# Optimization experiments

Measured on AMD Instinct MI355X. Metric: run time of the kernel, lower is better.

## Reference

```python
import jax, jax.numpy as jnp
import numpy as np

C = 64
N_H = 4
N_WIN = 16
WIN_L = 8   # compressor window length (overlapped)
WIN_S = 4   # compressor stride -> T//4 blocks


def _rms(x, eps=1e-6):
    return x * jax.lax.rsqrt(jnp.mean(x * x, axis=-1, keepdims=True) + eps)


def _rope(x, negate=False):
    # x: (..., L, D); rotate-half RoPE over positions 0..L-1
    L, D = x.shape[-2], x.shape[-1]
    half = D // 2
    inv_freq = 1.0 / (10000.0 ** (jnp.arange(half, dtype=x.dtype) / half))
    ang = jnp.arange(L, dtype=x.dtype)[:, None] * inv_freq  # (L, half)
    if negate:
        ang = -ang
    cos, sin = jnp.cos(ang), jnp.sin(ang)
    x1, x2 = x[..., :half], x[..., half:]
    return jnp.concatenate([x1 * cos - x2 * sin, x1 * sin + x2 * cos], axis=-1)


def _compress(H, W):
    # overlapped token compressor: windows of WIN_L, stride WIN_S, zero-pad tail
    B, T, d = H.shape
    Tc = T // WIN_S
    Hp = jnp.pad(H, ((0, 0), (0, WIN_L - WIN_S), (0, 0)))
    idx = WIN_S * jnp.arange(Tc)[:, None] + jnp.arange(WIN_L)[None, :]  # (Tc, WIN_L)
    win = Hp[:, idx]                       # (B, Tc, WIN_L, d)
    return win.reshape(B, Tc, WIN_L * d) @ W  # (B, Tc, out)


def setup_inputs() -> dict:
    key = jax.random.key(0)
    ks = jax.random.split(key, 11)
    B, T, d = 2, 2048, 256

    def w(k, shape, fan):
        return jax.random.normal(k, shape, jnp.float32) / np.float32(np.sqrt(fan))

    H = jax.random.normal(ks[0], (B, T, d), jnp.float32)
    return {
        'H': H,
        'Wc_comp': w(ks[1], (WIN_L * d, C), WIN_L * d),
        'Wc_idx': w(ks[2], (WIN_L * d, 32), WIN_L * d),
        'W_DQ': w(ks[3], (d, 64), d),
        'W_IUQ': w(ks[4], (64, 4 * 32), 64),
        'W_w': w(ks[5], (64, 4), 64),
        'W_Q': w(ks[6], (d, N_H * C), d),
        'W_KV': w(ks[7], (d, C), d),
        'g_q': jnp.ones((N_H, C), jnp.float32),
        'g_k': jnp.ones((C,), jnp.float32),
        'g_v': jnp.ones((C,), jnp.float32),
        'Wg0': w(ks[8], (2 * C, 64), 2 * C),
        'bg0': jnp.zeros((64,), jnp.float32),
        'Wg1': w(ks[9], (2 * C, 64), 2 * C),
        'bg1': jnp.zeros((64,), jnp.float32),
        'Wout': w(ks[10], (128, d), 128),
        'bout': jnp.zeros((d,), jnp.float32),
    }


def reference(H, Wc_comp, Wc_idx, W_DQ, W_IUQ, W_w, W_Q, W_KV,
              g_q, g_k, g_v, Wg0, bg0, Wg1, bg1, Wout, bout):
    B, T, d = H.shape
    Tc = T // 4
    k_top = min(8, Tc)

    # ---- lightning indexer ----
    H_dc = H @ W_DQ                                   # (B,T,64)
    Q_I = (H_dc @ W_IUQ).reshape(B, T, 4, 32)         # (B,T,4,32)
    W_Iw = (H_dc @ W_w)[..., None]                    # (B,T,4,1)
    K_I = _compress(H, Wc_idx)                        # (B,Tc,32)
    dot = jnp.einsum('bthc,bsc->bths', Q_I, K_I)      # (B,T,4,Tc)
    I_ts = (W_Iw * jax.nn.relu(dot)).sum(axis=2)      # (B,T,Tc)

    t = jnp.arange(T)[:, None]
    s = jnp.arange(Tc)[None, :]
    mask_I = jnp.where(4 * s <= t, 0.0, -jnp.inf)     # (T,Tc) causal over blocks
    _, topk_idx = jax.lax.top_k(I_ts + mask_I, k_top)  # (B,T,k)
    bI = jnp.arange(B)[:, None, None]
    tI = jnp.arange(T)[None, :, None]
    M_comp = jnp.full((B, T, Tc), -jnp.inf).at[bI, tI, topk_idx].set(0.0)

    # ---- compressed + sliding KV ----
    KV = jnp.concatenate([_compress(H, Wc_comp), H @ W_KV], axis=1)  # (B,Tc+T,C)

    Q = (H @ W_Q).reshape(B, T, N_H, C).transpose(0, 2, 1, 3)        # (B,nh,T,C)
    Q = _rms(Q) * g_q[None, :, None, :]
    K = _rms(KV) * g_k
    V = _rms(KV) * g_v
    Q = _rope(Q)
    K = _rope(K)
    V = _rope(V)

    S = jnp.einsum('bhtc,bsc->bhts', Q, K) / np.float32(np.sqrt(C))  # (B,nh,T,Tc+T)

    S_comp = S[..., :Tc] + M_comp[:, None]
    rel = t - jnp.arange(T)[None, :]
    mask_slide = jnp.where((rel >= 0) & (rel < N_WIN), 0.0, -jnp.inf)  # (T,T)
    S_slide = S[..., Tc:] + mask_slide

    P = jax.nn.softmax(jnp.concatenate([S_comp, S_slide], axis=-1), axis=-1)
    O = jnp.einsum('bhts,bsc->bhtc', P, V)            # (B,nh,T,C)
    O = _rope(O, negate=True)

    O0 = O[:, :2].transpose(0, 2, 1, 3).reshape(B, T, 2 * C)
    O1 = O[:, 2:].transpose(0, 2, 1, 3).reshape(B, T, 2 * C)
    p_all = jnp.concatenate([O0 @ Wg0 + bg0, O1 @ Wg1 + bg1], axis=-1)
    return p_all @ Wout + bout
```

## Files before the change

kernel.cpp:

```cpp
#include <hip/hip_runtime.h>
#include <math.h>

#define T_DIM 2048
#define B_DIM 2
#define D_DIM 256
#define TC 512
#define KV_LEN 2560

__device__ __forceinline__ float wave_sum64(float v) {
#pragma unroll
    for (int off = 32; off > 0; off >>= 1) v += __shfl_xor(v, off, 64);
    return v;
}

__device__ __forceinline__ float rope_angle(int pos, int j) {
    float inv = powf(10000.0f, -(float)j * (1.0f / 32.0f));
    return (float)pos * inv;
}

__global__ __launch_bounds__(256) void k_phase1(
    const float* __restrict__ H, const float* __restrict__ W_Q,
    const float* __restrict__ W_KV, const float* __restrict__ W_DQ,
    const float* __restrict__ W_IUQ, const float* __restrict__ W_w,
    const float* __restrict__ Wc_comp, const float* __restrict__ Wc_idx,
    const float* __restrict__ g_q, const float* __restrict__ g_k,
    const float* __restrict__ g_v,
    float* __restrict__ QI, float* __restrict__ Wiw, float* __restrict__ Qr,
    float* __restrict__ KIbuf, float* __restrict__ Kbuf, float* __restrict__ Vbuf)
{
    __shared__ float smem[8960];
    int tid = threadIdx.x;
    int lane = tid & 63;

    if (blockIdx.x < 512) {
        int bt0 = blockIdx.x * 8;
        float* sH = smem;
        float* sW = smem + 2048;
        float* sHdc = smem + 8192;
        float* sWw = smem + 8704;

        for (int i = tid; i < 512; i += 256) {
            int tok = i >> 6;
            int c4 = (i & 63) << 2;
            *(float4*)&sH[tok * 256 + c4] =
                *(const float4*)(H + ((size_t)(bt0 + tok) << 8) + c4);
        }

        int cg = lane;
        int tg = tid >> 6;
        float acc[2][6];
#pragma unroll
        for (int a = 0; a < 2; ++a)
#pragma unroll
            for (int m = 0; m < 6; ++m) acc[a][m] = 0.f;

        for (int kc = 0; kc < 16; ++kc) {
            __syncthreads();
            for (int i = tid; i < 1536; i += 256) {
                int r = i / 96;
                int cc = (i % 96) * 4;
                int gr = kc * 16 + r;
                float4 v;
                if (cc < 256)      v = *(const float4*)(W_Q + (size_t)gr * 256 + cc);
                else if (cc < 320) v = *(const float4*)(W_KV + (size_t)gr * 64 + (cc - 256));
                else               v = *(const float4*)(W_DQ + (size_t)gr * 64 + (cc - 320));
                *(float4*)&sW[r * 384 + cc] = v;
            }
            __syncthreads();
#pragma unroll
            for (int k = 0; k < 16; ++k) {
                float h0 = sH[(2 * tg) * 256 + kc * 16 + k];
                float h1 = sH[(2 * tg + 1) * 256 + kc * 16 + k];
#pragma unroll
                for (int m = 0; m < 6; ++m) {
                    float w = sW[k * 384 + cg + 64 * m];
                    acc[0][m] = fmaf(h0, w, acc[0][m]);
                    acc[1][m] = fmaf(h1, w, acc[1][m]);
                }
            }
        }

#pragma unroll
        for (int tt = 0; tt < 2; ++tt)
            sHdc[(2 * tg + tt) * 64 + lane] = acc[tt][5];
        __syncthreads();
        for (int i = tid * 4; i < 8192; i += 1024)
            *(float4*)&smem[i] = *(const float4*)(W_IUQ + i);
        if (tid < 64) ((float4*)sWw)[tid] = ((const float4*)W_w)[tid];
        __syncthreads();
        float* sWI = smem;

        int j = lane & 31;
#pragma unroll
        for (int tt = 0; tt < 2; ++tt) {
            int tok = 2 * tg + tt;
            int bt = bt0 + tok;
            int b = bt >> 11;
            int t = bt & 2047;

            float s_t, c_t;
            sincosf(rope_angle(t, j), &s_t, &c_t);

#pragma unroll
            for (int r = 0; r < 4; ++r) {
                float qv = acc[tt][r];
                float ss = wave_sum64(qv * qv);
                float sc = rsqrtf(ss * (1.0f / 64.0f) + 1e-6f);
                float q = qv * sc * g_q[r * 64 + lane];
                float prt = __shfl_xor(q, 32, 64);
                float o = (lane < 32) ? fmaf(q, c_t, -prt * s_t)
                                      : fmaf(prt, s_t, q * c_t);
                Qr[(size_t)bt * 256 + r * 64 + lane] = o;
            }
            {
                float kvv = acc[tt][4];
                float ss = wave_sum64(kvv * kvv);
                float sc = rsqrtf(ss * (1.0f / 64.0f) + 1e-6f);
                float kk = kvv * sc * g_k[lane];
                float vv = kvv * sc * g_v[lane];
                int pos = TC + t;
                float s_p, c_p;
                sincosf(rope_angle(pos, j), &s_p, &c_p);
                float pk = __shfl_xor(kk, 32, 64);
                float pv = __shfl_xor(vv, 32, 64);
                float ko = (lane < 32) ? fmaf(kk, c_p, -pk * s_p) : fmaf(pk, s_p, kk * c_p);
                float vo = (lane < 32) ? fmaf(vv, c_p, -pv * s_p) : fmaf(pv, s_p, vv * c_p);
                size_t off = ((size_t)b * KV_LEN + pos) * 64 + lane;
                Kbuf[off] = ko;
                Vbuf[off] = vo;
            }
            {
                float a0 = 0.f, a1 = 0.f;
#pragma unroll 8
                for (int jj = 0; jj < 64; ++jj) {
                    float hv = sHdc[tok * 64 + jj];
                    a0 = fmaf(hv, sWI[jj * 128 + lane], a0);
                    a1 = fmaf(hv, sWI[jj * 128 + 64 + lane], a1);
                }
                QI[(size_t)bt * 128 + lane] = a0;
                QI[(size_t)bt * 128 + 64 + lane] = a1;
                if (lane < 4) {
                    float aw = 0.f;
                    for (int jj = 0; jj < 64; ++jj)
                        aw = fmaf(sHdc[tok * 64 + jj], sWw[jj * 4 + lane], aw);
                    Wiw[(size_t)bt * 4 + lane] = aw;
                }
            }
        }
    } else {
        int cid = blockIdx.x - 512;
        int wv = tid >> 6;
        int b = cid >> 8;
        int s0 = (cid & 255) * 2;

        float* sA = smem;
        float* sRed = smem + 4096;
        float* sRedI = smem + 4608;

#pragma unroll
        for (int tt = 0; tt < 2; ++tt) {
#pragma unroll
            for (int rl = 0; rl < 2; ++rl) {
                int row = 4 * (s0 + tt) + 2 * wv + rl;
                float4 v = make_float4(0.f, 0.f, 0.f, 0.f);
                if (row < T_DIM)
                    v = *(const float4*)(H + ((size_t)b * T_DIM + row) * 256 + lane * 4);
                *(float4*)&sA[(tt * 4 + wv) * 512 + rl * 256 + lane * 4] = v;
            }
        }

        int k0 = wv * 512;
        float ac0 = 0.f, ac1 = 0.f;
        const float* Wc = Wc_comp + (size_t)k0 * 64 + lane;
        for (int k = 0; k < 512; k += 4) {
            float4 a0 = *(float4*)&sA[(0 * 4 + wv) * 512 + k];
            float4 a1 = *(float4*)&sA[(1 * 4 + wv) * 512 + k];
#pragma unroll
            for (int kk = 0; kk < 4; ++kk) {
                float w = Wc[(size_t)(k + kk) * 64];
                ac0 = fmaf(((const float*)&a0)[kk], w, ac0);
                ac1 = fmaf(((const float*)&a1)[kk], w, ac1);
            }
        }
        sRed[(wv * 2 + 0) * 64 + lane] = ac0;
        sRed[(wv * 2 + 1) * 64 + lane] = ac1;

        {
            int col = lane & 31;
            int half = lane >> 5;
            float ai0 = 0.f, ai1 = 0.f;
            const float* Wi = Wc_idx + (size_t)k0 * 32 + col;
            int kb = half * 256;
            for (int k = kb; k < kb + 256; k += 4) {
                float4 a0 = *(float4*)&sA[(0 * 4 + wv) * 512 + k];
                float4 a1 = *(float4*)&sA[(1 * 4 + wv) * 512 + k];
#pragma unroll
                for (int kk = 0; kk < 4; ++kk) {
                    float w = Wi[(size_t)(k + kk) * 32];
                    ai0 = fmaf(((const float*)&a0)[kk], w, ai0);
                    ai1 = fmaf(((const float*)&a1)[kk], w, ai1);
                }
            }
            ai0 += __shfl_xor(ai0, 32, 64);
            ai1 += __shfl_xor(ai1, 32, 64);
            if (lane < 32) {
                sRedI[(wv * 2 + 0) * 32 + lane] = ai0;
                sRedI[(wv * 2 + 1) * 32 + lane] = ai1;
            }
        }
        __syncthreads();

        if (wv < 2) {
            int tt = wv;
            int s = s0 + tt;
            float kvv = sRed[(0 * 2 + tt) * 64 + lane] + sRed[(1 * 2 + tt) * 64 + lane] +
                        sRed[(2 * 2 + tt) * 64 + lane] + sRed[(3 * 2 + tt) * 64 + lane];
            float ss = wave_sum64(kvv * kvv);
            float sc = rsqrtf(ss * (1.0f / 64.0f) + 1e-6f);
            float kk = kvv * sc * g_k[lane];
            float vv = kvv * sc * g_v[lane];
            int j = lane & 31;
            float sa, ca;
            sincosf(rope_angle(s, j), &sa, &ca);
            float pk = __shfl_xor(kk, 32, 64);
            float pv = __shfl_xor(vv, 32, 64);
            float ko = (lane < 32) ? fmaf(kk, ca, -pk * sa) : fmaf(pk, sa, kk * ca);
            float vo = (lane < 32) ? fmaf(vv, ca, -pv * sa) : fmaf(pv, sa, vv * ca);
            size_t off = ((size_t)b * KV_LEN + s) * 64 + lane;
            Kbuf[off] = ko;
            Vbuf[off] = vo;
        } else {
            int tt = wv - 2;
            int s = s0 + tt;
            if (lane < 32) {
                float a = sRedI[(0 * 2 + tt) * 32 + lane] + sRedI[(1 * 2 + tt) * 32 + lane] +
                          sRedI[(2 * 2 + tt) * 32 + lane] + sRedI[(3 * 2 + tt) * 32 + lane];
                KIbuf[((size_t)b * TC + s) * 32 + lane] = a;
            }
        }
    }
}

__global__ __launch_bounds__(256) void k_score_topk(
    const float* __restrict__ QI, const float* __restrict__ Wiw,
    const float* __restrict__ KIbuf, int* __restrict__ topk)
{
    int tid = threadIdx.x;
    int wv = tid >> 6;
    int lane = tid & 63;
    int bt0 = blockIdx.x * 4;
    int bt = bt0 + wv;
    int b = bt >> 11;
    int t = bt & 2047;

    __shared__ float sQ[4][128];
    __shared__ float sw[4][4];
    __shared__ float sKI[64 * 33];

    sQ[wv][lane] = QI[(size_t)bt * 128 + lane];
    sQ[wv][64 + lane] = QI[(size_t)bt * 128 + 64 + lane];
    if (lane < 4) sw[wv][lane] = Wiw[(size_t)bt * 4 + lane];

    const float* KIb = KIbuf + (size_t)b * TC * 32;
    int smax = t >> 2;
    int smax_blk = ((bt0 + 3) & 2047) >> 2;

    float vals[8];
#pragma unroll
    for (int r = 0; r < 8; ++r) vals[r] = -INFINITY;

    for (int r = 0; r < 8; ++r) {
        if (r * 64 > smax_blk) break;
        __syncthreads();
        for (int i = tid; i < 512; i += 256) {
            int row = i >> 3;
            int cseg = (i & 7) * 4;
            float4 v = *(const float4*)(KIb + (size_t)(r * 64 + row) * 32 + cseg);
            float* dst = &sKI[row * 33 + cseg];
            dst[0] = v.x; dst[1] = v.y; dst[2] = v.z; dst[3] = v.w;
        }
        __syncthreads();

        int s = r * 64 + lane;
        if (s <= smax) {
            float dd0 = 0.f, dd1 = 0.f, dd2 = 0.f, dd3 = 0.f;
#pragma unroll
            for (int c = 0; c < 32; ++c) {
                float kv = sKI[lane * 33 + c];
                dd0 = fmaf(sQ[wv][c], kv, dd0);
                dd1 = fmaf(sQ[wv][32 + c], kv, dd1);
                dd2 = fmaf(sQ[wv][64 + c], kv, dd2);
                dd3 = fmaf(sQ[wv][96 + c], kv, dd3);
            }
            vals[r] = sw[wv][0] * fmaxf(dd0, 0.f) + sw[wv][1] * fmaxf(dd1, 0.f) +
                      sw[wv][2] * fmaxf(dd2, 0.f) + sw[wv][3] * fmaxf(dd3, 0.f);
        }
    }

    unsigned consumed = 0u;
    for (int k2 = 0; k2 < 8; ++k2) {
        float bv = -INFINITY;
        int bi = 0x7fffffff;
#pragma unroll
        for (int r = 0; r < 8; ++r) {
            if (!(consumed & (1u << r))) {
                int s = lane + 64 * r;
                float v = vals[r];
                if (v > bv || (v == bv && s < bi)) { bv = v; bi = s; }
            }
        }
#pragma unroll
        for (int off = 1; off < 64; off <<= 1) {
            float ov = __shfl_xor(bv, off, 64);
            int oi = __shfl_xor(bi, off, 64);
            if (ov > bv || (ov == bv && oi < bi)) { bv = ov; bi = oi; }
        }
        if ((bi & 63) == lane) consumed |= 1u << (bi >> 6);
        if (lane == 0) topk[(size_t)bt * 8 + k2] = bi;
    }
}

__global__ __launch_bounds__(1024) void k_attn_out(
    const float* __restrict__ Qr, const float* __restrict__ Kbuf,
    const float* __restrict__ Vbuf, const int* __restrict__ topk,
    const float* __restrict__ Wg0, const float* __restrict__ bg0,
    const float* __restrict__ Wg1, const float* __restrict__ bg1,
    const float* __restrict__ Wout, const float* __restrict__ bout,
    float* __restrict__ out)
{
    int tid = threadIdx.x;
    int lt = tid >> 8;
    int t256 = tid & 255;
    int h = t256 >> 6;
    int lane = tid & 63;
    int bt = blockIdx.x * 4 + lt;
    int b = bt >> 11;
    int t = bt & 2047;

    __shared__ float sKV[4][48 * 65];
    __shared__ float sQ[4][256];
    __shared__ int sPos[4][24];
    __shared__ float sP[4][4][24];
    __shared__ float sO[4][256];
    __shared__ float sPall[4][128];

    sQ[lt][t256] = Qr[(size_t)bt * 256 + t256];
    if (t256 < 8) {
        sPos[lt][t256] = topk[(size_t)bt * 8 + t256];
    } else if (t256 < 24) {
        int rel = t256 - 8;
        int sp = t - rel;
        sPos[lt][t256] = (sp >= 0) ? (TC + sp) : -1;
    }
    __syncthreads();

    for (int i = t256; i < 768; i += 256) {
        int row = i >> 4;
        int seg = (i & 15) << 2;
        int key = (row < 24) ? row : row - 24;
        int pos = sPos[lt][key];
        if (pos >= 0) {
            const float* src = ((row < 24) ? Kbuf : Vbuf) +
                               ((size_t)b * KV_LEN + pos) * 64 + seg;
            float4 v = *(const float4*)src;
            float* dst = &sKV[lt][row * 65 + seg];
            dst[0] = v.x; dst[1] = v.y; dst[2] = v.z; dst[3] = v.w;
        }
    }
    __syncthreads();

    float scv = -INFINITY;
    if (lane < 24) {
        int pos = sPos[lt][lane];
        if (pos >= 0) {
            float dd = 0.f;
#pragma unroll
            for (int c = 0; c < 64; ++c)
                dd = fmaf(sQ[lt][h * 64 + c], sKV[lt][lane * 65 + c], dd);
            scv = dd * 0.125f;
        }
    }
    float m = scv;
#pragma unroll
    for (int off = 1; off < 64; off <<= 1) m = fmaxf(m, __shfl_xor(m, off, 64));
    float p = expf(scv - m);
    if (scv == -INFINITY) p = 0.f;
    float l = p;
#pragma unroll
    for (int off = 1; off < 64; off <<= 1) l += __shfl_xor(l, off, 64);
    p /= l;
    if (lane < 24) sP[lt][h][lane] = p;

    float o = 0.f;
#pragma unroll
    for (int j2 = 0; j2 < 24; ++j2) {
        int pos = sPos[lt][j2];
        if (pos >= 0)
            o = fmaf(sP[lt][h][j2], sKV[lt][(24 + j2) * 65 + lane], o);
    }

    int j = lane & 31;
    float sa, ca;
    sincosf(rope_angle(t, j), &sa, &ca);
    float prt = __shfl_xor(o, 32, 64);
    float oo = (lane < 32) ? fmaf(o, ca, prt * sa) : fmaf(-prt, sa, o * ca);
    sO[lt][h * 64 + lane] = oo;
    __syncthreads();

    if (t256 < 128) {
        float a;
        if (t256 < 64) {
            a = bg0[t256];
            for (int c = 0; c < 128; ++c) a = fmaf(sO[lt][c], Wg0[c * 64 + t256], a);
        } else {
            int i = t256 - 64;
            a = bg1[i];
            for (int c = 0; c < 128; ++c) a = fmaf(sO[lt][128 + c], Wg1[c * 64 + i], a);
        }
        sPall[lt][t256] = a;
    }
    __syncthreads();

    float a = bout[t256];
    for (int i = 0; i < 128; ++i) a = fmaf(sPall[lt][i], Wout[i * 256 + t256], a);
    out[(size_t)bt * 256 + t256] = a;
}

extern "C" void kernel_launch(void* const* d_in, const int* in_sizes, int n_in,
                              void* d_out, int out_size, void* d_ws, size_t ws_size,
                              hipStream_t stream) {
    const float* H       = (const float*)d_in[0];
    const float* Wc_comp = (const float*)d_in[1];
    const float* Wc_idx  = (const float*)d_in[2];
    const float* W_DQ    = (const float*)d_in[3];
    const float* W_IUQ   = (const float*)d_in[4];
    const float* W_w     = (const float*)d_in[5];
    const float* W_Q     = (const float*)d_in[6];
    const float* W_KV    = (const float*)d_in[7];
    const float* g_q     = (const float*)d_in[8];
    const float* g_k     = (const float*)d_in[9];
    const float* g_v     = (const float*)d_in[10];
    const float* Wg0     = (const float*)d_in[11];
    const float* bg0     = (const float*)d_in[12];
    const float* Wg1     = (const float*)d_in[13];
    const float* bg1     = (const float*)d_in[14];
    const float* Wout    = (const float*)d_in[15];
    const float* bout    = (const float*)d_in[16];

    float* ws  = (float*)d_ws;
    float* QI  = ws;
    float* Qr  = QI + 524288;
    float* Wiw = Qr + 1048576;
    float* KI  = Wiw + 16384;
    float* Kb  = KI + 32768;
    float* Vb  = Kb + 327680;
    int* topkb = (int*)(Vb + 327680);

    float* outp = (float*)d_out;

    hipLaunchKernelGGL(k_phase1, dim3(1024), dim3(256), 0, stream,
                       H, W_Q, W_KV, W_DQ, W_IUQ, W_w, Wc_comp, Wc_idx,
                       g_q, g_k, g_v, QI, Wiw, Qr, KI, Kb, Vb);
    hipLaunchKernelGGL(k_score_topk, dim3((B_DIM * T_DIM) / 4), dim3(256), 0, stream,
                       QI, Wiw, KI, topkb);
    hipLaunchKernelGGL(k_attn_out, dim3((B_DIM * T_DIM) / 4), dim3(1024), 0, stream,
                       Qr, Kb, Vb, topkb, Wg0, bg0, Wg1, bg1, Wout, bout, outp);
}
```

Before: 213.1 us.

## Process 16 tokens per phase-1 block and 4 compressed rows per compressor block

```diff
diff --git a/kernel.cpp b/kernel.cpp
--- a/kernel.cpp
+++ b/kernel.cpp
@@ -28,29 +28,28 @@
     float* __restrict__ QI, float* __restrict__ Wiw, float* __restrict__ Qr,
     float* __restrict__ KIbuf, float* __restrict__ Kbuf, float* __restrict__ Vbuf)
 {
-    __shared__ float smem[8960];
+    __shared__ float smem[12544];
     int tid = threadIdx.x;
     int lane = tid & 63;
-
-    if (blockIdx.x < 512) {
-        int bt0 = blockIdx.x * 8;
-        float* sH = smem;
-        float* sW = smem + 2048;
-        float* sHdc = smem + 8192;
-        float* sWw = smem + 8704;
-
-        for (int i = tid; i < 512; i += 256) {
-            int tok = i >> 6;
-            int c4 = (i & 63) << 2;
-            *(float4*)&sH[tok * 256 + c4] =
-                *(const float4*)(H + ((size_t)(bt0 + tok) << 8) + c4);
-        }
-
-        int cg = lane;
-        int tg = tid >> 6;
-        float acc[2][6];
-#pragma unroll
-        for (int a = 0; a < 2; ++a)
+    int wv = tid >> 6;
+
+    if (blockIdx.x < 256) {
+        int bt0 = blockIdx.x * 16;
+        float* sHT = smem;
+        float* sW  = smem + 5120;
+        float* sHdc = smem + 11264;
+        float* sWw = smem + 12288;
+
+#pragma unroll 4
+        for (int it = 0; it < 16; ++it) {
+            float v = H[((size_t)(bt0 + it)) * 256 + tid];
+            sHT[tid * 20 + it] = v;
+        }
+
+        int l = lane, tg = wv;
+        float acc[4][6];
+#pragma unroll
+        for (int a = 0; a < 4; ++a)
 #pragma unroll
             for (int m = 0; m < 6; ++m) acc[a][m] = 0.f;
 
@@ -69,20 +68,86 @@
             __syncthreads();
 #pragma unroll
             for (int k = 0; k < 16; ++k) {
-                float h0 = sH[(2 * tg) * 256 + kc * 16 + k];
-                float h1 = sH[(2 * tg + 1) * 256 + kc * 16 + k];
-#pragma unroll
-                for (int m = 0; m < 6; ++m) {
-                    float w = sW[k * 384 + cg + 64 * m];
-                    acc[0][m] = fmaf(h0, w, acc[0][m]);
-                    acc[1][m] = fmaf(h1, w, acc[1][m]);
+                float4 h4 = *(float4*)&sHT[(kc * 16 + k) * 20 + 4 * tg];
+                float2 w0 = *(float2*)&sW[k * 384 + 2 * l];
+                float2 w1 = *(float2*)&sW[k * 384 + 128 + 2 * l];
+                float2 w2 = *(float2*)&sW[k * 384 + 256 + 2 * l];
+                const float* hp = (const float*)&h4;
+#pragma unroll
+                for (int tt = 0; tt < 4; ++tt) {
+                    float h = hp[tt];
+                    acc[tt][0] = fmaf(h, w0.x, acc[tt][0]);
+                    acc[tt][1] = fmaf(h, w0.y, acc[tt][1]);
+                    acc[tt][2] = fmaf(h, w1.x, acc[tt][2]);
+                    acc[tt][3] = fmaf(h, w1.y, acc[tt][3]);
+                    acc[tt][4] = fmaf(h, w2.x, acc[tt][4]);
+                    acc[tt][5] = fmaf(h, w2.y, acc[tt][5]);
                 }
             }
         }
 
-#pragma unroll
-        for (int tt = 0; tt < 2; ++tt)
-            sHdc[(2 * tg + tt) * 64 + lane] = acc[tt][5];
+        int il = l & 31;
+        int half_hi = l >> 5;
+#pragma unroll
+        for (int tt = 0; tt < 4; ++tt) {
+            int tok = 4 * tg + tt;
+            int bt = bt0 + tok;
+            int b = bt >> 11;
+            int t = bt & 2047;
+            int j0 = 2 * (il & 15), j1 = j0 + 1;
+            float s0, c0, s1, c1;
+            sincosf(rope_angle(t, j0), &s0, &c0);
+            sincosf(rope_angle(t, j1), &s1, &c1);
+
+#pragma unroll
+            for (int mg = 0; mg < 2; ++mg) {
+                int h = mg * 2 + half_hi;
+                float a = acc[tt][2 * mg], bb = acc[tt][2 * mg + 1];
+                float ss = a * a + bb * bb;
+#pragma unroll
+                for (int off = 1; off <= 16; off <<= 1) ss += __shfl_xor(ss, off, 64);
+                float sc = rsqrtf(ss * (1.0f / 64.0f) + 1e-6f);
+                float qa = a * sc * g_q[h * 64 + 2 * il];
+                float qb = bb * sc * g_q[h * 64 + 2 * il + 1];
+                float pa = __shfl_xor(qa, 16, 64);
+                float pb = __shfl_xor(qb, 16, 64);
+                float oa, ob;
+                if (il < 16) { oa = fmaf(qa, c0, -pa * s0); ob = fmaf(qb, c1, -pb * s1); }
+                else         { oa = fmaf(pa, s0, qa * c0);  ob = fmaf(pb, s1, qb * c1); }
+                *(float2*)&Qr[(size_t)bt * 256 + h * 64 + 2 * il] = make_float2(oa, ob);
+            }
+
+            if (l < 32) {
+                float a = acc[tt][4], bb = acc[tt][5];
+                float ss = a * a + bb * bb;
+#pragma unroll
+                for (int off = 1; off <= 16; off <<= 1) ss += __shfl_xor(ss, off, 64);
+                float sc = rsqrtf(ss * (1.0f / 64.0f) + 1e-6f);
+                float ka = a * sc * g_k[2 * il], kb = bb * sc * g_k[2 * il + 1];
+                float va = a * sc * g_v[2 * il], vb = bb * sc * g_v[2 * il + 1];
+                int pos = TC + t;
+                float s0p, c0p, s1p, c1p;
+                sincosf(rope_angle(pos, j0), &s0p, &c0p);
+                sincosf(rope_angle(pos, j1), &s1p, &c1p);
+                float pka = __shfl_xor(ka, 16, 64), pkb = __shfl_xor(kb, 16, 64);
+                float pva = __shfl_xor(va, 16, 64), pvb = __shfl_xor(vb, 16, 64);
+                float koa, kob, voa, vob;
+                if (il < 16) {
+                    koa = fmaf(ka, c0p, -pka * s0p); kob = fmaf(kb, c1p, -pkb * s1p);
+                    voa = fmaf(va, c0p, -pva * s0p); vob = fmaf(vb, c1p, -pvb * s1p);
+                } else {
+                    koa = fmaf(pka, s0p, ka * c0p);  kob = fmaf(pkb, s1p, kb * c1p);
+                    voa = fmaf(pva, s0p, va * c0p);  vob = fmaf(pvb, s1p, vb * c1p);
+                }
+                size_t off2 = ((size_t)b * KV_LEN + pos) * 64 + 2 * il;
+                *(float2*)&Kbuf[off2] = make_float2(koa, kob);
+                *(float2*)&Vbuf[off2] = make_float2(voa, vob);
+            } else {
+                sHdc[tok * 64 + 2 * (l - 32)] = acc[tt][4];
+                sHdc[tok * 64 + 2 * (l - 32) + 1] = acc[tt][5];
+            }
+        }
+
         __syncthreads();
         for (int i = tid * 4; i < 8192; i += 1024)
             *(float4*)&smem[i] = *(const float4*)(W_IUQ + i);
@@ -90,75 +155,37 @@
         __syncthreads();
         float* sWI = smem;
 
-        int j = lane & 31;
-#pragma unroll
-        for (int tt = 0; tt < 2; ++tt) {
-            int tok = 2 * tg + tt;
+#pragma unroll
+        for (int tt = 0; tt < 4; ++tt) {
+            int tok = 4 * tg + tt;
             int bt = bt0 + tok;
-            int b = bt >> 11;
-            int t = bt & 2047;
-
-            float s_t, c_t;
-            sincosf(rope_angle(t, j), &s_t, &c_t);
-
-#pragma unroll
-            for (int r = 0; r < 4; ++r) {
-                float qv = acc[tt][r];
-                float ss = wave_sum64(qv * qv);
-                float sc = rsqrtf(ss * (1.0f / 64.0f) + 1e-6f);
-                float q = qv * sc * g_q[r * 64 + lane];
-                float prt = __shfl_xor(q, 32, 64);
-                float o = (lane < 32) ? fmaf(q, c_t, -prt * s_t)
-                                      : fmaf(prt, s_t, q * c_t);
-                Qr[(size_t)bt * 256 + r * 64 + lane] = o;
-            }
-            {
-                float kvv = acc[tt][4];
-                float ss = wave_sum64(kvv * kvv);
-                float sc = rsqrtf(ss * (1.0f / 64.0f) + 1e-6f);
-                float kk = kvv * sc * g_k[lane];
-                float vv = kvv * sc * g_v[lane];
-                int pos = TC + t;
-                float s_p, c_p;
-                sincosf(rope_angle(pos, j), &s_p, &c_p);
-                float pk = __shfl_xor(kk, 32, 64);
-                float pv = __shfl_xor(vv, 32, 64);
-                float ko = (lane < 32) ? fmaf(kk, c_p, -pk * s_p) : fmaf(pk, s_p, kk * c_p);
-                float vo = (lane < 32) ? fmaf(vv, c_p, -pv * s_p) : fmaf(pv, s_p, vv * c_p);
-                size_t off = ((size_t)b * KV_LEN + pos) * 64 + lane;
-                Kbuf[off] = ko;
-                Vbuf[off] = vo;
-            }
-            {
-                float a0 = 0.f, a1 = 0.f;
+            float a0 = 0.f, a1 = 0.f;
 #pragma unroll 8
-                for (int jj = 0; jj < 64; ++jj) {
-                    float hv = sHdc[tok * 64 + jj];
-                    a0 = fmaf(hv, sWI[jj * 128 + lane], a0);
-                    a1 = fmaf(hv, sWI[jj * 128 + 64 + lane], a1);
-                }
-                QI[(size_t)bt * 128 + lane] = a0;
-                QI[(size_t)bt * 128 + 64 + lane] = a1;
-                if (lane < 4) {
-                    float aw = 0.f;
-                    for (int jj = 0; jj < 64; ++jj)
-                        aw = fmaf(sHdc[tok * 64 + jj], sWw[jj * 4 + lane], aw);
-                    Wiw[(size_t)bt * 4 + lane] = aw;
-                }
+            for (int jj = 0; jj < 64; ++jj) {
+                float hv = sHdc[tok * 64 + jj];
+                a0 = fmaf(hv, sWI[jj * 128 + l], a0);
+                a1 = fmaf(hv, sWI[jj * 128 + 64 + l], a1);
+            }
+            QI[(size_t)bt * 128 + l] = a0;
+            QI[(size_t)bt * 128 + 64 + l] = a1;
+            if (l < 4) {
+                float aw = 0.f;
+                for (int jj = 0; jj < 64; ++jj)
+                    aw = fmaf(sHdc[tok * 64 + jj], sWw[jj * 4 + l], aw);
+                Wiw[(size_t)bt * 4 + l] = aw;
             }
         }
     } else {
-        int cid = blockIdx.x - 512;
-        int wv = tid >> 6;
-        int b = cid >> 8;
-        int s0 = (cid & 255) * 2;
+        int cid = blockIdx.x - 256;
+        int b = cid >> 7;
+        int s0 = (cid & 127) * 4;
 
         float* sA = smem;
-        float* sRed = smem + 4096;
-        float* sRedI = smem + 4608;
-
-#pragma unroll
-        for (int tt = 0; tt < 2; ++tt) {
+        float* sRed = smem + 8192;
+        float* sRedI = smem + 9216;
+
+#pragma unroll
+        for (int tt = 0; tt < 4; ++tt) {
 #pragma unroll
             for (int rl = 0; rl < 2; ++rl) {
                 int row = 4 * (s0 + tt) + 2 * wv + rl;
@@ -170,51 +197,58 @@
         }
 
         int k0 = wv * 512;
-        float ac0 = 0.f, ac1 = 0.f;
+        float ac[4] = {0.f, 0.f, 0.f, 0.f};
         const float* Wc = Wc_comp + (size_t)k0 * 64 + lane;
         for (int k = 0; k < 512; k += 4) {
             float4 a0 = *(float4*)&sA[(0 * 4 + wv) * 512 + k];
             float4 a1 = *(float4*)&sA[(1 * 4 + wv) * 512 + k];
+            float4 a2 = *(float4*)&sA[(2 * 4 + wv) * 512 + k];
+            float4 a3 = *(float4*)&sA[(3 * 4 + wv) * 512 + k];
 #pragma unroll
             for (int kk = 0; kk < 4; ++kk) {
                 float w = Wc[(size_t)(k + kk) * 64];
-                ac0 = fmaf(((const float*)&a0)[kk], w, ac0);
-                ac1 = fmaf(((const float*)&a1)[kk], w, ac1);
-            }
-        }
-        sRed[(wv * 2 + 0) * 64 + lane] = ac0;
-        sRed[(wv * 2 + 1) * 64 + lane] = ac1;
+                ac[0] = fmaf(((const float*)&a0)[kk], w, ac[0]);
+                ac[1] = fmaf(((const float*)&a1)[kk], w, ac[1]);
+                ac[2] = fmaf(((const float*)&a2)[kk], w, ac[2]);
+                ac[3] = fmaf(((const float*)&a3)[kk], w, ac[3]);
+            }
+        }
+#pragma unroll
+        for (int tt = 0; tt < 4; ++tt) sRed[(wv * 4 + tt) * 64 + lane] = ac[tt];
 
         {
             int col = lane & 31;
             int half = lane >> 5;
-            float ai0 = 0.f, ai1 = 0.f;
+            float ai[4] = {0.f, 0.f, 0.f, 0.f};
             const float* Wi = Wc_idx + (size_t)k0 * 32 + col;
             int kb = half * 256;
             for (int k = kb; k < kb + 256; k += 4) {
                 float4 a0 = *(float4*)&sA[(0 * 4 + wv) * 512 + k];
                 float4 a1 = *(float4*)&sA[(1 * 4 + wv) * 512 + k];
+                float4 a2 = *(float4*)&sA[(2 * 4 + wv) * 512 + k];
+                float4 a3 = *(float4*)&sA[(3 * 4 + wv) * 512 + k];
 #pragma unroll
                 for (int kk = 0; kk < 4; ++kk) {
                     float w = Wi[(size_t)(k + kk) * 32];
-                    ai0 = fmaf(((const float*)&a0)[kk], w, ai0);
-                    ai1 = fmaf(((const float*)&a1)[kk], w, ai1);
+                    ai[0] = fmaf(((const float*)&a0)[kk], w, ai[0]);
+                    ai[1] = fmaf(((const float*)&a1)[kk], w, ai[1]);
+                    ai[2] = fmaf(((const float*)&a2)[kk], w, ai[2]);
+                    ai[3] = fmaf(((const float*)&a3)[kk], w, ai[3]);
                 }
             }
-            ai0 += __shfl_xor(ai0, 32, 64);
-            ai1 += __shfl_xor(ai1, 32, 64);
-            if (lane < 32) {
-                sRedI[(wv * 2 + 0) * 32 + lane] = ai0;
-                sRedI[(wv * 2 + 1) * 32 + lane] = ai1;
+#pragma unroll
+            for (int tt = 0; tt < 4; ++tt) {
+                ai[tt] += __shfl_xor(ai[tt], 32, 64);
+                if (lane < 32) sRedI[(wv * 4 + tt) * 32 + lane] = ai[tt];
             }
         }
         __syncthreads();
 
-        if (wv < 2) {
+        {
             int tt = wv;
             int s = s0 + tt;
-            float kvv = sRed[(0 * 2 + tt) * 64 + lane] + sRed[(1 * 2 + tt) * 64 + lane] +
-                        sRed[(2 * 2 + tt) * 64 + lane] + sRed[(3 * 2 + tt) * 64 + lane];
+            float kvv = sRed[(0 * 4 + tt) * 64 + lane] + sRed[(1 * 4 + tt) * 64 + lane] +
+                        sRed[(2 * 4 + tt) * 64 + lane] + sRed[(3 * 4 + tt) * 64 + lane];
             float ss = wave_sum64(kvv * kvv);
             float sc = rsqrtf(ss * (1.0f / 64.0f) + 1e-6f);
             float kk = kvv * sc * g_k[lane];
@@ -229,12 +263,9 @@
             size_t off = ((size_t)b * KV_LEN + s) * 64 + lane;
             Kbuf[off] = ko;
             Vbuf[off] = vo;
-        } else {
-            int tt = wv - 2;
-            int s = s0 + tt;
             if (lane < 32) {
-                float a = sRedI[(0 * 2 + tt) * 32 + lane] + sRedI[(1 * 2 + tt) * 32 + lane] +
-                          sRedI[(2 * 2 + tt) * 32 + lane] + sRedI[(3 * 2 + tt) * 32 + lane];
+                float a = sRedI[(0 * 4 + tt) * 32 + lane] + sRedI[(1 * 4 + tt) * 32 + lane] +
+                          sRedI[(2 * 4 + tt) * 32 + lane] + sRedI[(3 * 4 + tt) * 32 + lane];
                 KIbuf[((size_t)b * TC + s) * 32 + lane] = a;
             }
         }
@@ -458,7 +489,7 @@
 
     float* outp = (float*)d_out;
 
-    hipLaunchKernelGGL(k_phase1, dim3(1024), dim3(256), 0, stream,
+    hipLaunchKernelGGL(k_phase1, dim3(512), dim3(256), 0, stream,
                        H, W_Q, W_KV, W_DQ, W_IUQ, W_w, Wc_comp, Wc_idx,
                        g_q, g_k, g_v, QI, Wiw, Qr, KI, Kb, Vb);
     hipLaunchKernelGGL(k_score_topk, dim3((B_DIM * T_DIM) / 4), dim3(256), 0, stream,
```

Measured after the change: 215.6 us. About the same (+1.1%).

## Run projection and compressor GEMMs on bf16 MFMA with split-precision operands

Applied to the files above, without the earlier changes.

```diff
diff --git a/kernel.cpp b/kernel.cpp
--- a/kernel.cpp
+++ b/kernel.cpp
@@ -1,4 +1,5 @@
 #include <hip/hip_runtime.h>
+#include <hip/hip_bf16.h>
 #include <math.h>
 
 #define T_DIM 2048
@@ -6,6 +7,10 @@
 #define D_DIM 256
 #define TC 512
 #define KV_LEN 2560
+#define HPAD 2056
+
+typedef __attribute__((ext_vector_type(8))) short bf16x8;
+typedef __attribute__((ext_vector_type(4))) float f32x4;
 
 __device__ __forceinline__ float wave_sum64(float v) {
 #pragma unroll
@@ -18,226 +23,279 @@
     return (float)pos * inv;
 }
 
-__global__ __launch_bounds__(256) void k_phase1(
+__device__ __forceinline__ unsigned short f2bf_hi(float x) {
+    __hip_bfloat16 h = __float2bfloat16(x);
+    return *(unsigned short*)&h;
+}
+
+__global__ __launch_bounds__(256) void k_prep(
     const float* __restrict__ H, const float* __restrict__ W_Q,
     const float* __restrict__ W_KV, const float* __restrict__ W_DQ,
-    const float* __restrict__ W_IUQ, const float* __restrict__ W_w,
     const float* __restrict__ Wc_comp, const float* __restrict__ Wc_idx,
-    const float* __restrict__ g_q, const float* __restrict__ g_k,
+    unsigned short* __restrict__ Hp_hi, unsigned short* __restrict__ Hp_lo,
+    unsigned short* __restrict__ Bpt, unsigned short* __restrict__ Bct)
+{
+    int gtid = blockIdx.x * 256 + threadIdx.x;
+    int gstride = gridDim.x * 256;
+
+    for (int i = gtid; i < B_DIM * HPAD * 256; i += gstride) {
+        int b = i / (HPAD * 256);
+        int rem = i - b * (HPAD * 256);
+        int row = rem >> 8;
+        int col = rem & 255;
+        float x = (row < T_DIM) ? H[((size_t)b * T_DIM + row) * 256 + col] : 0.f;
+        unsigned short hi = f2bf_hi(x);
+        __hip_bfloat16 hb = *(__hip_bfloat16*)&hi;
+        float hif = __bfloat162float(hb);
+        unsigned short lo = f2bf_hi(x - hif);
+        Hp_hi[i] = hi;
+        Hp_lo[i] = lo;
+    }
+
+    for (int i = gtid; i < 384 * 768; i += gstride) {
+        int n = i / 768;
+        int kp = i - n * 768;
+        int k = kp & 255;
+        float w;
+        if (n < 256)      w = W_Q[(size_t)k * 256 + n];
+        else if (n < 320) w = W_KV[(size_t)k * 64 + (n - 256)];
+        else              w = W_DQ[(size_t)k * 64 + (n - 320)];
+        unsigned short hi = f2bf_hi(w);
+        __hip_bfloat16 hb = *(__hip_bfloat16*)&hi;
+        unsigned short lo = f2bf_hi(w - __bfloat162float(hb));
+        Bpt[i] = (kp >= 256 && kp < 512) ? lo : hi;
+    }
+
+    for (int i = gtid; i < 96 * 6144; i += gstride) {
+        int n = i / 6144;
+        int kp = i - n * 6144;
+        int k = kp & 2047;
+        float w = (n < 64) ? Wc_comp[(size_t)k * 64 + n]
+                           : Wc_idx[(size_t)k * 32 + (n - 64)];
+        unsigned short hi = f2bf_hi(w);
+        __hip_bfloat16 hb = *(__hip_bfloat16*)&hi;
+        unsigned short lo = f2bf_hi(w - __bfloat162float(hb));
+        Bct[i] = (kp >= 2048 && kp < 4096) ? lo : hi;
+    }
+}
+
+__global__ __launch_bounds__(256) void k_mfma(
+    const unsigned short* __restrict__ Hp_hi, const unsigned short* __restrict__ Hp_lo,
+    const unsigned short* __restrict__ Bpt, const unsigned short* __restrict__ Bct,
+    float* __restrict__ Pre, float* __restrict__ Prec_part)
+{
+    int tid = threadIdx.x;
+    int w = tid >> 6;
+    int lane = tid & 63;
+    int mrow = lane & 15;
+    int q = lane >> 4;
+
+    if (blockIdx.x < 64) {
+        int bt0 = blockIdx.x * 64;
+        int b = bt0 >> 11;
+        int t0 = bt0 & 2047;
+        int n0 = w * 96;
+
+        f32x4 acc[4][6];
+#pragma unroll
+        for (int mt = 0; mt < 4; ++mt)
+#pragma unroll
+            for (int nt = 0; nt < 6; ++nt) acc[mt][nt] = (f32x4){0.f, 0.f, 0.f, 0.f};
+
+        const size_t abase = (size_t)(b * HPAD + t0 + mrow) * 256;
+
+        for (int ks = 0; ks < 24; ++ks) {
+            int seg = ks >> 3;
+            int kk = 32 * (ks & 7) + 8 * q;
+            const unsigned short* Asrc = (seg < 2 ? Hp_hi : Hp_lo);
+            int kp = 32 * ks + 8 * q;
+
+            bf16x8 af[4];
+#pragma unroll
+            for (int mt = 0; mt < 4; ++mt)
+                af[mt] = *(const bf16x8*)(Asrc + abase + (size_t)(16 * mt) * 256 + kk);
+            bf16x8 bfb[6];
+#pragma unroll
+            for (int nt = 0; nt < 6; ++nt)
+                bfb[nt] = *(const bf16x8*)(Bpt + (size_t)(n0 + 16 * nt + mrow) * 768 + kp);
+#pragma unroll
+            for (int mt = 0; mt < 4; ++mt)
+#pragma unroll
+                for (int nt = 0; nt < 6; ++nt)
+                    acc[mt][nt] = __builtin_amdgcn_mfma_f32_16x16x32_bf16(
+                        af[mt], bfb[nt], acc[mt][nt], 0, 0, 0);
+        }
+
+#pragma unroll
+        for (int mt = 0; mt < 4; ++mt)
+#pragma unroll
+            for (int nt = 0; nt < 6; ++nt)
+#pragma unroll
+                for (int reg = 0; reg < 4; ++reg)
+                    Pre[(size_t)(bt0 + 16 * mt + 4 * q + reg) * 384 + n0 + 16 * nt + mrow] =
+                        acc[mt][nt][reg];
+    } else {
+        int cid = blockIdx.x - 64;
+        int m0 = cid * 64;
+        int b = m0 >> 9;
+        int s0 = m0 & 511;
+        int kw = w * 1536;
+
+        f32x4 acc[4][6];
+#pragma unroll
+        for (int mt = 0; mt < 4; ++mt)
+#pragma unroll
+            for (int nt = 0; nt < 6; ++nt) acc[mt][nt] = (f32x4){0.f, 0.f, 0.f, 0.f};
+
+        for (int ks = 0; ks < 48; ++ks) {
+            int kp = kw + 32 * ks + 8 * q;
+            int seg = kp >> 11;
+            int kk = kp & 2047;
+            int row_off = kk >> 8;
+            int kcol = kk & 255;
+            const unsigned short* Asrc = (seg < 2 ? Hp_hi : Hp_lo);
+
+            bf16x8 af[4];
+#pragma unroll
+            for (int mt = 0; mt < 4; ++mt) {
+                int m = s0 + 16 * mt + mrow;
+                af[mt] = *(const bf16x8*)(Asrc + (size_t)(b * HPAD + 4 * m + row_off) * 256 + kcol);
+            }
+            bf16x8 bfb[6];
+#pragma unroll
+            for (int nt = 0; nt < 6; ++nt)
+                bfb[nt] = *(const bf16x8*)(Bct + (size_t)(16 * nt + mrow) * 6144 + kp);
+#pragma unroll
+            for (int mt = 0; mt < 4; ++mt)
+#pragma unroll
+                for (int nt = 0; nt < 6; ++nt)
+                    acc[mt][nt] = __builtin_amdgcn_mfma_f32_16x16x32_bf16(
+                        af[mt], bfb[nt], acc[mt][nt], 0, 0, 0);
+        }
+
+        float* dst = Prec_part + (size_t)w * (1024 * 96);
+#pragma unroll
+        for (int mt = 0; mt < 4; ++mt)
+#pragma unroll
+            for (int nt = 0; nt < 6; ++nt)
+#pragma unroll
+                for (int reg = 0; reg < 4; ++reg)
+                    dst[(size_t)(m0 + 16 * mt + 4 * q + reg) * 96 + 16 * nt + mrow] =
+                        acc[mt][nt][reg];
+    }
+}
+
+__global__ __launch_bounds__(256) void k_epi_proj(
+    const float* __restrict__ Pre, const float* __restrict__ W_IUQ,
+    const float* __restrict__ W_w, const float* __restrict__ g_q,
+    const float* __restrict__ g_k, const float* __restrict__ g_v,
+    float* __restrict__ QI, float* __restrict__ Wiw, float* __restrict__ Qr,
+    float* __restrict__ Kbuf, float* __restrict__ Vbuf)
+{
+    int tid = threadIdx.x;
+    int wv = tid >> 6;
+    int lane = tid & 63;
+    int bt = blockIdx.x * 4 + wv;
+    int b = bt >> 11;
+    int t = bt & 2047;
+
+    __shared__ float sWI[8192];
+    __shared__ float sWw[256];
+    __shared__ float sHdc[4][64];
+
+    for (int i = tid * 4; i < 8192; i += 1024)
+        *(float4*)&sWI[i] = *(const float4*)(W_IUQ + i);
+    if (tid < 64) ((float4*)sWw)[tid] = ((const float4*)W_w)[tid];
+
+    const float* pr = Pre + (size_t)bt * 384;
+    sHdc[wv][lane] = pr[320 + lane];
+    __syncthreads();
+
+    int j = lane & 31;
+    float s_t, c_t;
+    sincosf(rope_angle(t, j), &s_t, &c_t);
+
+#pragma unroll
+    for (int r = 0; r < 4; ++r) {
+        float qv = pr[r * 64 + lane];
+        float ss = wave_sum64(qv * qv);
+        float sc = rsqrtf(ss * (1.0f / 64.0f) + 1e-6f);
+        float qq = qv * sc * g_q[r * 64 + lane];
+        float prt = __shfl_xor(qq, 32, 64);
+        float o = (lane < 32) ? fmaf(qq, c_t, -prt * s_t)
+                              : fmaf(prt, s_t, qq * c_t);
+        Qr[(size_t)bt * 256 + r * 64 + lane] = o;
+    }
+    {
+        float kvv = pr[256 + lane];
+        float ss = wave_sum64(kvv * kvv);
+        float sc = rsqrtf(ss * (1.0f / 64.0f) + 1e-6f);
+        float kk = kvv * sc * g_k[lane];
+        float vv = kvv * sc * g_v[lane];
+        int pos = TC + t;
+        float s_p, c_p;
+        sincosf(rope_angle(pos, j), &s_p, &c_p);
+        float pk = __shfl_xor(kk, 32, 64);
+        float pv = __shfl_xor(vv, 32, 64);
+        float ko = (lane < 32) ? fmaf(kk, c_p, -pk * s_p) : fmaf(pk, s_p, kk * c_p);
+        float vo = (lane < 32) ? fmaf(vv, c_p, -pv * s_p) : fmaf(pv, s_p, vv * c_p);
+        size_t off = ((size_t)b * KV_LEN + pos) * 64 + lane;
+        Kbuf[off] = ko;
+        Vbuf[off] = vo;
+    }
+    {
+        float a0 = 0.f, a1 = 0.f;
+#pragma unroll 8
+        for (int jj = 0; jj < 64; ++jj) {
+            float hv = sHdc[wv][jj];
+            a0 = fmaf(hv, sWI[jj * 128 + lane], a0);
+            a1 = fmaf(hv, sWI[jj * 128 + 64 + lane], a1);
+        }
+        QI[(size_t)bt * 128 + lane] = a0;
+        QI[(size_t)bt * 128 + 64 + lane] = a1;
+        if (lane < 4) {
+            float aw = 0.f;
+            for (int jj = 0; jj < 64; ++jj)
+                aw = fmaf(sHdc[wv][jj], sWw[jj * 4 + lane], aw);
+            Wiw[(size_t)bt * 4 + lane] = aw;
+        }
+    }
+}
+
+__global__ __launch_bounds__(256) void k_epi_comp(
+    const float* __restrict__ Prec_part, const float* __restrict__ g_k,
     const float* __restrict__ g_v,
-    float* __restrict__ QI, float* __restrict__ Wiw, float* __restrict__ Qr,
     float* __restrict__ KIbuf, float* __restrict__ Kbuf, float* __restrict__ Vbuf)
 {
-    __shared__ float smem[8960];
     int tid = threadIdx.x;
+    int wv = tid >> 6;
     int lane = tid & 63;
-
-    if (blockIdx.x < 512) {
-        int bt0 = blockIdx.x * 8;
-        float* sH = smem;
-        float* sW = smem + 2048;
-        float* sHdc = smem + 8192;
-        float* sWw = smem + 8704;
-
-        for (int i = tid; i < 512; i += 256) {
-            int tok = i >> 6;
-            int c4 = (i & 63) << 2;
-            *(float4*)&sH[tok * 256 + c4] =
-                *(const float4*)(H + ((size_t)(bt0 + tok) << 8) + c4);
-        }
-
-        int cg = lane;
-        int tg = tid >> 6;
-        float acc[2][6];
-#pragma unroll
-        for (int a = 0; a < 2; ++a)
-#pragma unroll
-            for (int m = 0; m < 6; ++m) acc[a][m] = 0.f;
-
-        for (int kc = 0; kc < 16; ++kc) {
-            __syncthreads();
-            for (int i = tid; i < 1536; i += 256) {
-                int r = i / 96;
-                int cc = (i % 96) * 4;
-                int gr = kc * 16 + r;
-                float4 v;
-                if (cc < 256)      v = *(const float4*)(W_Q + (size_t)gr * 256 + cc);
-                else if (cc < 320) v = *(const float4*)(W_KV + (size_t)gr * 64 + (cc - 256));
-                else               v = *(const float4*)(W_DQ + (size_t)gr * 64 + (cc - 320));
-                *(float4*)&sW[r * 384 + cc] = v;
-            }
-            __syncthreads();
-#pragma unroll
-            for (int k = 0; k < 16; ++k) {
-                float h0 = sH[(2 * tg) * 256 + kc * 16 + k];
-                float h1 = sH[(2 * tg + 1) * 256 + kc * 16 + k];
-#pragma unroll
-                for (int m = 0; m < 6; ++m) {
-                    float w = sW[k * 384 + cg + 64 * m];
-                    acc[0][m] = fmaf(h0, w, acc[0][m]);
-                    acc[1][m] = fmaf(h1, w, acc[1][m]);
-                }
-            }
-        }
-
-#pragma unroll
-        for (int tt = 0; tt < 2; ++tt)
-            sHdc[(2 * tg + tt) * 64 + lane] = acc[tt][5];
-        __syncthreads();
-        for (int i = tid * 4; i < 8192; i += 1024)
-            *(float4*)&smem[i] = *(const float4*)(W_IUQ + i);
-        if (tid < 64) ((float4*)sWw)[tid] = ((const float4*)W_w)[tid];
-        __syncthreads();
-        float* sWI = smem;
-
-        int j = lane & 31;
-#pragma unroll
-        for (int tt = 0; tt < 2; ++tt) {
-            int tok = 2 * tg + tt;
-            int bt = bt0 + tok;
-            int b = bt >> 11;
-            int t = bt & 2047;
-
-            float s_t, c_t;
-            sincosf(rope_angle(t, j), &s_t, &c_t);
-
-#pragma unroll
-            for (int r = 0; r < 4; ++r) {
-                float qv = acc[tt][r];
-                float ss = wave_sum64(qv * qv);
-                float sc = rsqrtf(ss * (1.0f / 64.0f) + 1e-6f);
-                float q = qv * sc * g_q[r * 64 + lane];
-                float prt = __shfl_xor(q, 32, 64);
-                float o = (lane < 32) ? fmaf(q, c_t, -prt * s_t)
-                                      : fmaf(prt, s_t, q * c_t);
-                Qr[(size_t)bt * 256 + r * 64 + lane] = o;
-            }
-            {
-                float kvv = acc[tt][4];
-                float ss = wave_sum64(kvv * kvv);
-                float sc = rsqrtf(ss * (1.0f / 64.0f) + 1e-6f);
-                float kk = kvv * sc * g_k[lane];
-                float vv = kvv * sc * g_v[lane];
-                int pos = TC + t;
-                float s_p, c_p;
-                sincosf(rope_angle(pos, j), &s_p, &c_p);
-                float pk = __shfl_xor(kk, 32, 64);
-                float pv = __shfl_xor(vv, 32, 64);
-                float ko = (lane < 32) ? fmaf(kk, c_p, -pk * s_p) : fmaf(pk, s_p, kk * c_p);
-                float vo = (lane < 32) ? fmaf(vv, c_p, -pv * s_p) : fmaf(pv, s_p, vv * c_p);
-                size_t off = ((size_t)b * KV_LEN + pos) * 64 + lane;
-                Kbuf[off] = ko;
-                Vbuf[off] = vo;
-            }
-            {
-                float a0 = 0.f, a1 = 0.f;
-#pragma unroll 8
-                for (int jj = 0; jj < 64; ++jj) {
-                    float hv = sHdc[tok * 64 + jj];
-                    a0 = fmaf(hv, sWI[jj * 128 + lane], a0);
-                    a1 = fmaf(hv, sWI[jj * 128 + 64 + lane], a1);
-                }
-                QI[(size_t)bt * 128 + lane] = a0;
-                QI[(size_t)bt * 128 + 64 + lane] = a1;
-                if (lane < 4) {
-                    float aw = 0.f;
-                    for (int jj = 0; jj < 64; ++jj)
-                        aw = fmaf(sHdc[tok * 64 + jj], sWw[jj * 4 + lane], aw);
-                    Wiw[(size_t)bt * 4 + lane] = aw;
-                }
-            }
-        }
-    } else {
-        int cid = blockIdx.x - 512;
-        int wv = tid >> 6;
-        int b = cid >> 8;
-        int s0 = (cid & 255) * 2;
-
-        float* sA = smem;
-        float* sRed = smem + 4096;
-        float* sRedI = smem + 4608;
-
-#pragma unroll
-        for (int tt = 0; tt < 2; ++tt) {
-#pragma unroll
-            for (int rl = 0; rl < 2; ++rl) {
-                int row = 4 * (s0 + tt) + 2 * wv + rl;
-                float4 v = make_float4(0.f, 0.f, 0.f, 0.f);
-                if (row < T_DIM)
-                    v = *(const float4*)(H + ((size_t)b * T_DIM + row) * 256 + lane * 4);
-                *(float4*)&sA[(tt * 4 + wv) * 512 + rl * 256 + lane * 4] = v;
-            }
-        }
-
-        int k0 = wv * 512;
-        float ac0 = 0.f, ac1 = 0.f;
-        const float* Wc = Wc_comp + (size_t)k0 * 64 + lane;
-        for (int k = 0; k < 512; k += 4) {
-            float4 a0 = *(float4*)&sA[(0 * 4 + wv) * 512 + k];
-            float4 a1 = *(float4*)&sA[(1 * 4 + wv) * 512 + k];
-#pragma unroll
-            for (int kk = 0; kk < 4; ++kk) {
-                float w = Wc[(size_t)(k + kk) * 64];
-                ac0 = fmaf(((const float*)&a0)[kk], w, ac0);
-                ac1 = fmaf(((const float*)&a1)[kk], w, ac1);
-            }
-        }
-        sRed[(wv * 2 + 0) * 64 + lane] = ac0;
-        sRed[(wv * 2 + 1) * 64 + lane] = ac1;
-
-        {
-            int col = lane & 31;
-            int half = lane >> 5;
-            float ai0 = 0.f, ai1 = 0.f;
-            const float* Wi = Wc_idx + (size_t)k0 * 32 + col;
-            int kb = half * 256;
-            for (int k = kb; k < kb + 256; k += 4) {
-                float4 a0 = *(float4*)&sA[(0 * 4 + wv) * 512 + k];
-                float4 a1 = *(float4*)&sA[(1 * 4 + wv) * 512 + k];
-#pragma unroll
-                for (int kk = 0; kk < 4; ++kk) {
-                    float w = Wi[(size_t)(k + kk) * 32];
-                    ai0 = fmaf(((const float*)&a0)[kk], w, ai0);
-                    ai1 = fmaf(((const float*)&a1)[kk], w, ai1);
-                }
-            }
-            ai0 += __shfl_xor(ai0, 32, 64);
-            ai1 += __shfl_xor(ai1, 32, 64);
-            if (lane < 32) {
-                sRedI[(wv * 2 + 0) * 32 + lane] = ai0;
-                sRedI[(wv * 2 + 1) * 32 + lane] = ai1;
-            }
-        }
-        __syncthreads();
-
-        if (wv < 2) {
-            int tt = wv;
-            int s = s0 + tt;
-            float kvv = sRed[(0 * 2 + tt) * 64 + lane] + sRed[(1 * 2 + tt) * 64 + lane] +
-                        sRed[(2 * 2 + tt) * 64 + lane] + sRed[(3 * 2 + tt) * 64 + lane];
-            float ss = wave_sum64(kvv * kvv);
-            float sc = rsqrtf(ss * (1.0f / 64.0f) + 1e-6f);
-            float kk = kvv * sc * g_k[lane];
-            float vv = kvv * sc * g_v[lane];
-            int j = lane & 31;
-            float sa, ca;
-            sincosf(rope_angle(s, j), &sa, &ca);
-            float pk = __shfl_xor(kk, 32, 64);
-            float pv = __shfl_xor(vv, 32, 64);
-            float ko = (lane < 32) ? fmaf(kk, ca, -pk * sa) : fmaf(pk, sa, kk * ca);
-            float vo = (lane < 32) ? fmaf(vv, ca, -pv * sa) : fmaf(pv, sa, vv * ca);
-            size_t off = ((size_t)b * KV_LEN + s) * 64 + lane;
-            Kbuf[off] = ko;
-            Vbuf[off] = vo;
-        } else {
-            int tt = wv - 2;
-            int s = s0 + tt;
-            if (lane < 32) {
-                float a = sRedI[(0 * 2 + tt) * 32 + lane] + sRedI[(1 * 2 + tt) * 32 + lane] +
-                          sRedI[(2 * 2 + tt) * 32 + lane] + sRedI[(3 * 2 + tt) * 32 + lane];
-                KIbuf[((size_t)b * TC + s) * 32 + lane] = a;
-            }
-        }
+    int sg = blockIdx.x * 4 + wv;
+    int b = sg >> 9;
+    int s = sg & 511;
+
+    const float* p0 = Prec_part + (size_t)sg * 96;
+    float kvv = p0[lane] + p0[98304 + lane] + p0[2 * 98304 + lane] + p0[3 * 98304 + lane];
+
+    float ss = wave_sum64(kvv * kvv);
+    float sc = rsqrtf(ss * (1.0f / 64.0f) + 1e-6f);
+    float kk = kvv * sc * g_k[lane];
+    float vv = kvv * sc * g_v[lane];
+    int j = lane & 31;
+    float sa, ca;
+    sincosf(rope_angle(s, j), &sa, &ca);
+    float pk = __shfl_xor(kk, 32, 64);
+    float pv = __shfl_xor(vv, 32, 64);
+    float ko = (lane < 32) ? fmaf(kk, ca, -pk * sa) : fmaf(pk, sa, kk * ca);
+    float vo = (lane < 32) ? fmaf(vv, ca, -pv * sa) : fmaf(pv, sa, vv * ca);
+    size_t off = ((size_t)b * KV_LEN + s) * 64 + lane;
+    Kbuf[off] = ko;
+    Vbuf[off] = vo;
+
+    if (lane < 32) {
+        float a = p0[64 + lane] + p0[98304 + 64 + lane] +
+                  p0[2 * 98304 + 64 + lane] + p0[3 * 98304 + 64 + lane];
+        KIbuf[((size_t)b * TC + s) * 32 + lane] = a;
     }
 }
 
@@ -448,19 +506,30 @@
     const float* bout    = (const float*)d_in[16];
 
     float* ws  = (float*)d_ws;
-    float* QI  = ws;
-    float* Qr  = QI + 524288;
-    float* Wiw = Qr + 1048576;
-    float* KI  = Wiw + 16384;
-    float* Kb  = KI + 32768;
-    float* Vb  = Kb + 327680;
-    int* topkb = (int*)(Vb + 327680);
+    float* QI   = ws;
+    float* Qr   = ws + 524288;
+    float* Wiw  = ws + 1572864;
+    float* KI   = ws + 1589248;
+    float* Kb   = ws + 1622016;
+    float* Vb   = ws + 1949696;
+    int*   topkb = (int*)(ws + 2277376);
+    float* Pre  = ws + 2310144;
+    float* Prec = ws + 3883008;
+    unsigned short* Hp_hi = (unsigned short*)(ws + 4276224);
+    unsigned short* Hp_lo = (unsigned short*)(ws + 4802560);
+    unsigned short* Bpt   = (unsigned short*)(ws + 5328896);
+    unsigned short* Bct   = (unsigned short*)(ws + 5476352);
 
     float* outp = (float*)d_out;
 
-    hipLaunchKernelGGL(k_phase1, dim3(1024), dim3(256), 0, stream,
-                       H, W_Q, W_KV, W_DQ, W_IUQ, W_w, Wc_comp, Wc_idx,
-                       g_q, g_k, g_v, QI, Wiw, Qr, KI, Kb, Vb);
+    hipLaunchKernelGGL(k_prep, dim3(512), dim3(256), 0, stream,
+                       H, W_Q, W_KV, W_DQ, Wc_comp, Wc_idx, Hp_hi, Hp_lo, Bpt, Bct);
+    hipLaunchKernelGGL(k_mfma, dim3(80), dim3(256), 0, stream,
+                       Hp_hi, Hp_lo, Bpt, Bct, Pre, Prec);
+    hipLaunchKernelGGL(k_epi_proj, dim3(1024), dim3(256), 0, stream,
+                       Pre, W_IUQ, W_w, g_q, g_k, g_v, QI, Wiw, Qr, Kb, Vb);
+    hipLaunchKernelGGL(k_epi_comp, dim3(256), dim3(256), 0, stream,
+                       Prec, g_k, g_v, KI, Kb, Vb);
     hipLaunchKernelGGL(k_score_topk, dim3((B_DIM * T_DIM) / 4), dim3(256), 0, stream,
                        QI, Wiw, KI, topkb);
     hipLaunchKernelGGL(k_attn_out, dim3((B_DIM * T_DIM) / 4), dim3(1024), 0, stream,
```

After: 230.7 us. 1.08x slower.
